# Optimization experiments

Hardware: AMD Instinct MI355X
Metric: run time of the kernel (lower is better)

## Reference

```python
import jax, jax.numpy as jnp
import numpy as np


def _segment_softmax(x, seg, num_segments):
    # x: (E, C), seg: (E,) int. Numerically stable per-segment softmax along dim 0.
    m = jax.ops.segment_max(x, seg, num_segments=num_segments)  # (S, C)
    # Guard empty segments (-inf) so gather stays finite for used rows.
    e = jnp.exp(x - m[seg])                                     # (E, C)
    s = jax.ops.segment_sum(e, seg, num_segments=num_segments)  # (S, C)
    return e / s[seg]


def setup_inputs() -> dict:
    key = jax.random.key(0)
    k1, k2, k3, k4 = jax.random.split(key, 4)
    E, C, S = 16777216, 2, 4096
    return {
        "xab": jax.random.normal(k1, (E, C), dtype=jnp.float32),
        "xba": jax.random.normal(k2, (E, C), dtype=jnp.float32),
        "src_id": jax.random.randint(k3, (E,), 0, S, dtype=jnp.int64),
        "tar_id": jax.random.randint(k4, (E,), 0, S, dtype=jnp.int64),
        "num_segments": S,
    }


def reference(xab, xba, src_id, tar_id, num_segments):
    zab = _segment_softmax(xab, src_id, num_segments)  # softmax over src groups
    zba = _segment_softmax(xba, tar_id, num_segments)  # softmax over tar groups
    return (zab * zba, zab, zba)
```

## Files before the change

### kernel.cpp

```cpp
#include <hip/hip_runtime.h>

#define NSEG 4096
#define QSCALE 131072.0f
#define QINV   (1.0f / 131072.0f)

typedef unsigned long long u64;
typedef unsigned int u32;
typedef float f32x4 __attribute__((ext_vector_type(4)));
typedef float f32x2 __attribute__((ext_vector_type(2)));

__global__ __launch_bounds__(1024, 8) void dsp_reduce(
    const f32x4* __restrict__ xab4, const f32x4* __restrict__ xba4,
    const int2* __restrict__ src2, const int2* __restrict__ tar2,
    float* __restrict__ partials,
    float* __restrict__ gtab,
    int Eh)
{
    __shared__ u64 ls[2 * NSEG];
    for (int i = threadIdx.x; i < 2 * NSEG; i += 1024) ls[i] = 0ull;
    __syncthreads();

    const int stride = gridDim.x * 1024;
    for (int u = blockIdx.x * 1024 + threadIdx.x; u < Eh; u += stride) {
        f32x4 a = xab4[u];
        f32x4 b = xba4[u];
        int2 s = src2[u];
        int2 t = tar2[u];

        u32 a0 = __float2uint_rn(__expf(a.x) * QSCALE);
        u32 a1 = __float2uint_rn(__expf(a.y) * QSCALE);
        u32 a2 = __float2uint_rn(__expf(a.z) * QSCALE);
        u32 a3 = __float2uint_rn(__expf(a.w) * QSCALE);
        atomicAdd(&ls[s.x], (u64)a0 | ((u64)a1 << 32));
        atomicAdd(&ls[s.y], (u64)a2 | ((u64)a3 << 32));

        u32 b0 = __float2uint_rn(__expf(b.x) * QSCALE);
        u32 b1 = __float2uint_rn(__expf(b.y) * QSCALE);
        u32 b2 = __float2uint_rn(__expf(b.z) * QSCALE);
        u32 b3 = __float2uint_rn(__expf(b.w) * QSCALE);
        atomicAdd(&ls[NSEG + t.x], (u64)b0 | ((u64)b1 << 32));
        atomicAdd(&ls[NSEG + t.y], (u64)b2 | ((u64)b3 << 32));
    }
    __syncthreads();

    if (partials) {
        float* dst = partials + (size_t)blockIdx.x * (4 * NSEG);
        for (int i = threadIdx.x; i < 2 * NSEG; i += 1024) {
            u64 v = ls[i];
            dst[2 * i]     = (float)(u32)v * QINV;
            dst[2 * i + 1] = (float)(u32)(v >> 32) * QINV;
        }
    } else {
        for (int i = threadIdx.x; i < 2 * NSEG; i += 1024) {
            u64 v = ls[i];
            float lo = (float)(u32)v * QINV;
            float hi = (float)(u32)(v >> 32) * QINV;
            if (lo != 0.f) atomicAdd(&gtab[2 * i], lo);
            if (hi != 0.f) atomicAdd(&gtab[2 * i + 1], hi);
        }
    }
}

__global__ __launch_bounds__(256) void dsp_sum(
    const f32x4* __restrict__ partials, f32x4* __restrict__ rcp_out, int nb)
{
    int i = blockIdx.x * blockDim.x + threadIdx.x;
    f32x4 acc = {0.f, 0.f, 0.f, 0.f};
    for (int p = 0; p < nb; ++p) {
        f32x4 v = __builtin_nontemporal_load(&partials[(size_t)p * NSEG + i]);
        acc += v;
    }
    f32x4 r;
    r.x = (acc.x > 0.f) ? 1.f / acc.x : 0.f;
    r.y = (acc.y > 0.f) ? 1.f / acc.y : 0.f;
    r.z = (acc.z > 0.f) ? 1.f / acc.z : 0.f;
    r.w = (acc.w > 0.f) ? 1.f / acc.w : 0.f;
    rcp_out[i] = r;
}

__global__ void dsp_rcp(float* __restrict__ sums, int n)
{
    int i = blockIdx.x * blockDim.x + threadIdx.x;
    if (i < n) {
        float v = sums[i];
        sums[i] = (v > 0.f) ? 1.f / v : 0.f;
    }
}

__global__ __launch_bounds__(256) void dsp_norm(
    const f32x4* __restrict__ xab4, const f32x4* __restrict__ xba4,
    const int2* __restrict__ src2, const int2* __restrict__ tar2,
    const f32x2* __restrict__ rcp_ab, const f32x2* __restrict__ rcp_ba,
    f32x4* __restrict__ out, int Eh)
{
    const int stride = gridDim.x * blockDim.x;
    for (int u = blockIdx.x * blockDim.x + threadIdx.x; u < Eh; u += stride) {
        f32x4 a = __builtin_nontemporal_load(&xab4[u]);
        f32x4 b = __builtin_nontemporal_load(&xba4[u]);
        int2 s = src2[u];
        int2 t = tar2[u];
        f32x2 ra0 = rcp_ab[s.x], ra1 = rcp_ab[s.y];
        f32x2 rb0 = rcp_ba[t.x], rb1 = rcp_ba[t.y];

        f32x4 zab = { __expf(a.x) * ra0.x, __expf(a.y) * ra0.y,
                      __expf(a.z) * ra1.x, __expf(a.w) * ra1.y };
        f32x4 zba = { __expf(b.x) * rb0.x, __expf(b.y) * rb0.y,
                      __expf(b.z) * rb1.x, __expf(b.w) * rb1.y };
        f32x4 prod = zab * zba;

        __builtin_nontemporal_store(prod, &out[u]);
        __builtin_nontemporal_store(zab,  &out[Eh + u]);
        __builtin_nontemporal_store(zba,  &out[2 * Eh + u]);
    }
}

extern "C" void kernel_launch(void* const* d_in, const int* in_sizes, int n_in,
                              void* d_out, int out_size, void* d_ws, size_t ws_size,
                              hipStream_t stream)
{
    const int E  = in_sizes[0] / 2;
    const int Eh = E / 2;
    const f32x4* xab4 = (const f32x4*)d_in[0];
    const f32x4* xba4 = (const f32x4*)d_in[1];
    const int2*  src2 = (const int2*)d_in[2];
    const int2*  tar2 = (const int2*)d_in[3];

    const int NB = 512;
    float* rcp_tab  = (float*)d_ws;
    float* partials = (float*)((char*)d_ws + 65536);
    size_t need = 65536 + (size_t)NB * 65536;

    if (ws_size >= need) {
        dsp_reduce<<<NB, 1024, 0, stream>>>(xab4, xba4, src2, tar2,
                                            partials, nullptr, Eh);
        dsp_sum<<<NSEG / 256, 256, 0, stream>>>((const f32x4*)partials,
                                                (f32x4*)rcp_tab, NB);
    } else {
        (void)hipMemsetAsync(d_ws, 0, 65536, stream);
        dsp_reduce<<<NB, 1024, 0, stream>>>(xab4, xba4, src2, tar2,
                                            nullptr, rcp_tab, Eh);
        dsp_rcp<<<64, 256, 0, stream>>>(rcp_tab, 4 * NSEG);
    }

    dsp_norm<<<2048, 256, 0, stream>>>(xab4, xba4, src2, tar2,
                                       (const f32x2*)rcp_tab,
                                       (const f32x2*)(rcp_tab + 2 * NSEG),
                                       (f32x4*)d_out, Eh);
}
```

Before: 408.6 us.

## Software-prefetch next iteration and stage reciprocal table in LDS for normalize

Both the reduce and normalize kernels now load the next grid-stride element before processing the current one. The aim is to overlap global memory latency with the exp and atomic work. The normalize kernel copies the 64KB reciprocal table into shared memory and reads it from there instead of doing scattered global gathers, and it now launches as 512 blocks of 1024 threads. The partials write is vectorized to float2, and the reduce kernel drops its min-blocks launch-bounds hint, which changes register allocation. The trade-off is higher register pressure from the prefetch and 64KB of LDS per normalize block, which limits occupancy.

After: 356.8 us. 1.15x faster.

```diff
diff --git a/kernel.cpp b/kernel.cpp
--- a/kernel.cpp
+++ b/kernel.cpp
@@ -9,7 +9,7 @@
 typedef float f32x4 __attribute__((ext_vector_type(4)));
 typedef float f32x2 __attribute__((ext_vector_type(2)));
 
-__global__ __launch_bounds__(1024, 8) void dsp_reduce(
+__global__ __launch_bounds__(1024) void dsp_reduce(
     const f32x4* __restrict__ xab4, const f32x4* __restrict__ xba4,
     const int2* __restrict__ src2, const int2* __restrict__ tar2,
     float* __restrict__ partials,
@@ -21,11 +21,15 @@
     __syncthreads();
 
     const int stride = gridDim.x * 1024;
-    for (int u = blockIdx.x * 1024 + threadIdx.x; u < Eh; u += stride) {
-        f32x4 a = xab4[u];
-        f32x4 b = xba4[u];
-        int2 s = src2[u];
-        int2 t = tar2[u];
+    int u = blockIdx.x * 1024 + threadIdx.x;
+
+    f32x4 a, b; int2 s, t;
+    if (u < Eh) { a = xab4[u]; b = xba4[u]; s = src2[u]; t = tar2[u]; }
+
+    while (u < Eh) {
+        int un = u + stride;
+        f32x4 an, bn; int2 sn, tn;
+        if (un < Eh) { an = xab4[un]; bn = xba4[un]; sn = src2[un]; tn = tar2[un]; }
 
         u32 a0 = __float2uint_rn(__expf(a.x) * QSCALE);
         u32 a1 = __float2uint_rn(__expf(a.y) * QSCALE);
@@ -40,15 +44,17 @@
         u32 b3 = __float2uint_rn(__expf(b.w) * QSCALE);
         atomicAdd(&ls[NSEG + t.x], (u64)b0 | ((u64)b1 << 32));
         atomicAdd(&ls[NSEG + t.y], (u64)b2 | ((u64)b3 << 32));
+
+        u = un; a = an; b = bn; s = sn; t = tn;
     }
     __syncthreads();
 
     if (partials) {
-        float* dst = partials + (size_t)blockIdx.x * (4 * NSEG);
+        f32x2* dst = (f32x2*)(partials + (size_t)blockIdx.x * (4 * NSEG));
         for (int i = threadIdx.x; i < 2 * NSEG; i += 1024) {
             u64 v = ls[i];
-            dst[2 * i]     = (float)(u32)v * QINV;
-            dst[2 * i + 1] = (float)(u32)(v >> 32) * QINV;
+            f32x2 w = { (float)(u32)v * QINV, (float)(u32)(v >> 32) * QINV };
+            dst[i] = w;
         }
     } else {
         for (int i = threadIdx.x; i < 2 * NSEG; i += 1024) {
@@ -87,20 +93,32 @@
     }
 }
 
-__global__ __launch_bounds__(256) void dsp_norm(
+__global__ __launch_bounds__(1024) void dsp_norm(
     const f32x4* __restrict__ xab4, const f32x4* __restrict__ xba4,
     const int2* __restrict__ src2, const int2* __restrict__ tar2,
-    const f32x2* __restrict__ rcp_ab, const f32x2* __restrict__ rcp_ba,
+    const f32x4* __restrict__ rcp_tab,
     f32x4* __restrict__ out, int Eh)
 {
-    const int stride = gridDim.x * blockDim.x;
-    for (int u = blockIdx.x * blockDim.x + threadIdx.x; u < Eh; u += stride) {
-        f32x4 a = __builtin_nontemporal_load(&xab4[u]);
-        f32x4 b = __builtin_nontemporal_load(&xba4[u]);
-        int2 s = src2[u];
-        int2 t = tar2[u];
-        f32x2 ra0 = rcp_ab[s.x], ra1 = rcp_ab[s.y];
-        f32x2 rb0 = rcp_ba[t.x], rb1 = rcp_ba[t.y];
+    __shared__ float ls[4 * NSEG];
+    for (int i = threadIdx.x; i < NSEG; i += 1024)
+        ((f32x4*)ls)[i] = rcp_tab[i];
+    __syncthreads();
+
+    const int stride = gridDim.x * 1024;
+    int u = blockIdx.x * 1024 + threadIdx.x;
+
+    f32x4 a, b; int2 s, t;
+    if (u < Eh) { a = xab4[u]; b = xba4[u]; s = src2[u]; t = tar2[u]; }
+
+    while (u < Eh) {
+        int un = u + stride;
+        f32x4 an, bn; int2 sn, tn;
+        if (un < Eh) { an = xab4[un]; bn = xba4[un]; sn = src2[un]; tn = tar2[un]; }
+
+        f32x2 ra0 = *(const f32x2*)&ls[2 * s.x];
+        f32x2 ra1 = *(const f32x2*)&ls[2 * s.y];
+        f32x2 rb0 = *(const f32x2*)&ls[2 * NSEG + 2 * t.x];
+        f32x2 rb1 = *(const f32x2*)&ls[2 * NSEG + 2 * t.y];
 
         f32x4 zab = { __expf(a.x) * ra0.x, __expf(a.y) * ra0.y,
                       __expf(a.z) * ra1.x, __expf(a.w) * ra1.y };
@@ -111,6 +129,8 @@
         __builtin_nontemporal_store(prod, &out[u]);
         __builtin_nontemporal_store(zab,  &out[Eh + u]);
         __builtin_nontemporal_store(zba,  &out[2 * Eh + u]);
+
+        u = un; a = an; b = bn; s = sn; t = tn;
     }
 }
 
@@ -142,8 +162,7 @@
         dsp_rcp<<<64, 256, 0, stream>>>(rcp_tab, 4 * NSEG);
     }
 
-    dsp_norm<<<2048, 256, 0, stream>>>(xab4, xba4, src2, tar2,
-                                       (const f32x2*)rcp_tab,
-                                       (const f32x2*)(rcp_tab + 2 * NSEG),
+    dsp_norm<<<512, 1024, 0, stream>>>(xab4, xba4, src2, tar2,
+                                       (const f32x4*)rcp_tab,
                                        (f32x4*)d_out, Eh);
 }
```
